# Performance work log

Hardware: AMD Instinct MI355X
Metric: run time of the kernel (lower is better)

The kernel has to match this reference:

```python
import math
import jax, jax.numpy as jnp
import numpy as np

# ---- hyperparams (match init_kwargs) ----
N_LEVELS = 16
F = 2                      # n_features_per_level
LOG2_T = 19                # log2_hashmap_size
BASE_RES = 16
PER_LEVEL_SCALE = 1.5
N_POINTS = 2 ** 21


def _aligned_level_size(res):
    return min(((res * res + 7) // 8) * 8, 1 << LOG2_T)

# static per-level resolution / offset tables (Python ints, mirror torch __init__)
RES, OFFS = [], []
_off = 0
_log2s = math.log2(PER_LEVEL_SCALE)
for _l in range(N_LEVELS):
    _scale = 2.0 ** (_l * _log2s) * BASE_RES - 1.0
    _r = int(math.ceil(_scale) + 1)
    RES.append(_r)
    OFFS.append(_off)
    _off += _aligned_level_size(_r)
TOTAL = _off
SIZES = [(OFFS[l + 1] - OFFS[l]) if l + 1 < N_LEVELS else TOTAL - OFFS[l]
         for l in range(N_LEVELS)]


def setup_inputs() -> dict:
    key = jax.random.key(0)
    k1, k2 = jax.random.split(key)
    # scale to [0, 0.95) so all 4 corner indices stay in-range on dense levels
    xy = jax.random.uniform(k1, (N_POINTS, 2), jnp.float32) * 0.95
    params = jax.random.uniform(k2, (TOTAL * F,), jnp.float32,
                                minval=-1e-4, maxval=1e-4)
    return {"xy": xy, "params": params}


def _grid_index(gx, gy, res, hsize):
    if hsize >= res * res:            # dense level
        return gx + gy * res
    # coherent prime hash in uint32 arithmetic (wraps == & 0xFFFFFFFF)
    h = (gx.astype(jnp.uint32) ^ (gy.astype(jnp.uint32) * jnp.uint32(2654435761)))
    return (h % jnp.uint32(hsize)).astype(jnp.int32)


def reference(xy, params):
    table = params.reshape(TOTAL, F)          # [TOTAL, F]
    outs = []
    for l in range(N_LEVELS):                 # small static loop over levels
        res, off, hsize = RES[l], OFFS[l], SIZES[l]
        pos = xy * (res - 1.0) + 0.5          # [N, 2]
        pg = jnp.floor(pos)
        frac = pos - pg
        pg = pg.astype(jnp.int32)
        gx0, gy0 = pg[:, 0], pg[:, 1]
        gx1, gy1 = gx0 + 1, gy0 + 1
        wx, wy = frac[:, 0:1], frac[:, 1:2]   # [N, 1]
        i00 = off + _grid_index(gx0, gy0, res, hsize)
        i10 = off + _grid_index(gx1, gy0, res, hsize)
        i01 = off + _grid_index(gx0, gy1, res, hsize)
        i11 = off + _grid_index(gx1, gy1, res, hsize)
        f00 = jnp.take(table, i00, axis=0)    # [N, F]
        f10 = jnp.take(table, i10, axis=0)
        f01 = jnp.take(table, i01, axis=0)
        f11 = jnp.take(table, i11, axis=0)
        out_l = (f00 * ((1.0 - wx) * (1.0 - wy))
                 + f10 * (wx * (1.0 - wy))
                 + f01 * ((1.0 - wx) * wy)
                 + f11 * (wx * wy))
        outs.append(out_l)
    return jnp.concatenate(outs, axis=-1)     # [N, N_LEVELS * F]
```

## Files before the change

kernel.cpp:

```cpp
#include <hip/hip_runtime.h>
#include <math.h>

#define N_LEVELS 16
#define NPTS (1 << 21)

typedef float vfloat4 __attribute__((ext_vector_type(4)));
typedef float vfloat2 __attribute__((ext_vector_type(2)));

struct LevelP {
    float scale;
    int   res;
    int   off;
    unsigned int mask;
    int   is_hash;
};
struct LevelTable { LevelP lv[N_LEVELS]; };
struct LevelMap   { int m[8][2]; };

__global__ __launch_bounds__(256) void enc_level_kernel(
        const float2* __restrict__ xy,
        const float*  __restrict__ table,
        float2* __restrict__ ws,
        LevelTable lt, LevelMap lm)
{
    int xcd   = blockIdx.x & 7;
    int slot  = blockIdx.x >> 3;
    int lvl   = lm.m[xcd][slot >> 10];
    int chunk = slot & 1023;

    const LevelP lp = lt.lv[lvl];
    const float2* tb = (const float2*)table + lp.off;
    float2* wsl = ws + (size_t)lvl * NPTS;

    int base = chunk * 2048 + threadIdx.x;

    #pragma unroll
    for (int i = 0; i < 8; ++i) {
        int p = base + i * 256;
        float2 pt = xy[p];

        float px = __fadd_rn(__fmul_rn(pt.x, lp.scale), 0.5f);
        float py = __fadd_rn(__fmul_rn(pt.y, lp.scale), 0.5f);
        float fx = floorf(px), fy = floorf(py);
        float wx = __fsub_rn(px, fx), wy = __fsub_rn(py, fy);
        int gx = (int)fx, gy = (int)fy;

        int i00, i10, i01, i11;
        if (lp.is_hash) {
            const unsigned K1 = 2654435761u;
            unsigned ux = (unsigned)gx, uy = (unsigned)gy;
            unsigned hy0 = uy * K1, hy1 = (uy + 1u) * K1;
            i00 = (int)((ux        ^ hy0) & lp.mask);
            i10 = (int)(((ux + 1u) ^ hy0) & lp.mask);
            i01 = (int)((ux        ^ hy1) & lp.mask);
            i11 = (int)(((ux + 1u) ^ hy1) & lp.mask);
        } else {
            i00 = gx + gy * lp.res;
            i10 = i00 + 1;
            i01 = i00 + lp.res;
            i11 = i01 + 1;
        }

        float2 f00 = tb[i00];
        float2 f10 = tb[i10];
        float2 f01 = tb[i01];
        float2 f11 = tb[i11];

        float owx = 1.0f - wx, owy = 1.0f - wy;
        float w00 = owx * owy, w10 = wx * owy, w01 = owx * wy, w11 = wx * wy;
        vfloat2 o;
        o.x = f00.x * w00 + f10.x * w10 + f01.x * w01 + f11.x * w11;
        o.y = f00.y * w00 + f10.y * w10 + f01.y * w01 + f11.y * w11;

        __builtin_nontemporal_store(o, (vfloat2*)&wsl[p]);
    }
}

__global__ __launch_bounds__(256) void interleave_kernel(
        const float2* __restrict__ ws,
        float4* __restrict__ out)
{
    int tid  = blockIdx.x * 256 + threadIdx.x;
    int pair = tid & 7;
    int p    = tid >> 3;

    const vfloat2* a = (const vfloat2*)(ws + (size_t)(2 * pair)     * NPTS);
    const vfloat2* b = (const vfloat2*)(ws + (size_t)(2 * pair + 1) * NPTS);
    vfloat2 va = __builtin_nontemporal_load(&a[p]);
    vfloat2 vb = __builtin_nontemporal_load(&b[p]);

    vfloat4 o = { va.x, va.y, vb.x, vb.y };
    __builtin_nontemporal_store(o, (vfloat4*)&out[(size_t)p * 8 + pair]);
}

__global__ __launch_bounds__(256) void hashenc_kernel(
        const float2* __restrict__ xy,
        const float*  __restrict__ table,
        float4* __restrict__ out,
        LevelTable lt)
{
    int tid  = blockIdx.x * 256 + threadIdx.x;
    int pair = tid & 7;
    int p    = tid >> 3;

    float2 pt = xy[p];
    float4 o;

    #pragma unroll
    for (int k = 0; k < 2; ++k) {
        const LevelP lp = lt.lv[2 * pair + k];
        float px = __fadd_rn(__fmul_rn(pt.x, lp.scale), 0.5f);
        float py = __fadd_rn(__fmul_rn(pt.y, lp.scale), 0.5f);
        float fx = floorf(px), fy = floorf(py);
        float wx = __fsub_rn(px, fx), wy = __fsub_rn(py, fy);
        int gx = (int)fx, gy = (int)fy;

        int i00, i10, i01, i11;
        if (lp.is_hash) {
            const unsigned K1 = 2654435761u;
            unsigned ux = (unsigned)gx, uy = (unsigned)gy;
            unsigned hy0 = uy * K1, hy1 = (uy + 1u) * K1;
            i00 = (int)((ux        ^ hy0) & lp.mask);
            i10 = (int)(((ux + 1u) ^ hy0) & lp.mask);
            i01 = (int)((ux        ^ hy1) & lp.mask);
            i11 = (int)(((ux + 1u) ^ hy1) & lp.mask);
        } else {
            i00 = gx + gy * lp.res;
            i10 = i00 + 1;
            i01 = i00 + lp.res;
            i11 = i01 + 1;
        }

        const float2* tb = (const float2*)table + lp.off;
        float2 f00 = tb[i00];
        float2 f10 = tb[i10];
        float2 f01 = tb[i01];
        float2 f11 = tb[i11];

        float owx = 1.0f - wx, owy = 1.0f - wy;
        float w00 = owx * owy, w10 = wx * owy, w01 = owx * wy, w11 = wx * wy;
        float ox = f00.x * w00 + f10.x * w10 + f01.x * w01 + f11.x * w11;
        float oy = f00.y * w00 + f10.y * w10 + f01.y * w01 + f11.y * w11;

        if (k == 0) { o.x = ox; o.y = oy; }
        else        { o.z = ox; o.w = oy; }
    }

    vfloat4 ov = { o.x, o.y, o.z, o.w };
    __builtin_nontemporal_store(ov, (vfloat4*)&out[(size_t)p * 8 + pair]);
}

extern "C" void kernel_launch(void* const* d_in, const int* in_sizes, int n_in,
                              void* d_out, int out_size, void* d_ws, size_t ws_size,
                              hipStream_t stream) {
    const float2* xy     = (const float2*)d_in[0];
    const float*  params = (const float*)d_in[1];
    float4*       out    = (float4*)d_out;

    LevelTable lt;
    double log2s = log2(1.5);
    long offs[N_LEVELS];
    int  res_arr[N_LEVELS];
    long off = 0;
    for (int l = 0; l < N_LEVELS; ++l) {
        double scale = pow(2.0, (double)l * log2s) * 16.0 - 1.0;
        int r = (int)ceil(scale) + 1;
        res_arr[l] = r;
        offs[l] = off;
        long sz = ((long)r * r + 7) / 8 * 8;
        if (sz > (1L << 19)) sz = 1L << 19;
        off += sz;
    }
    for (int l = 0; l < N_LEVELS; ++l) {
        long hsize = ((l + 1 < N_LEVELS) ? offs[l + 1] : off) - offs[l];
        long r2 = (long)res_arr[l] * res_arr[l];
        int is_hash = hsize < r2;
        lt.lv[l].scale   = (float)(res_arr[l] - 1);
        lt.lv[l].res     = res_arr[l];
        lt.lv[l].off     = (int)offs[l];
        lt.lv[l].is_hash = is_hash;
        lt.lv[l].mask    = is_hash ? (unsigned)(hsize - 1) : 0u;
    }

    size_t ws_needed = (size_t)N_LEVELS * NPTS * 2 * sizeof(float);
    if (ws_size >= ws_needed) {
        LevelMap lm;
        int map[8][2] = { {10,0},{11,1},{12,2},{13,3},{14,4},{15,5},{6,7},{8,9} };
        for (int x = 0; x < 8; ++x) { lm.m[x][0] = map[x][0]; lm.m[x][1] = map[x][1]; }

        float2* ws = (float2*)d_ws;
        dim3 gridA(16384), block(256);
        hipLaunchKernelGGL(enc_level_kernel, gridA, block, 0, stream,
                           xy, params, ws, lt, lm);
        dim3 gridB((NPTS * 8) / 256);
        hipLaunchKernelGGL(interleave_kernel, gridB, block, 0, stream,
                           (const float2*)ws, out);
    } else {
        long total_threads = (long)NPTS * 8;
        dim3 grid((unsigned)(total_threads / 256)), block(256);
        hipLaunchKernelGGL(hashenc_kernel, grid, block, 0, stream,
                           xy, params, out, lt);
    }
}
```

Measured before the change: 771.7 us.

## Batch gathers in encoder and stage interleave through LDS with coalesced loads

The per-level encoder now computes indices for four points at a time, then issues all sixteen table gathers before interpolating, which raises memory-level parallelism per thread. The interleave kernel now has each block read 256 points for all 16 levels with coalesced loads into padded shared memory, then write the interleaved output contiguously. The old version used strided 8-byte reads per thread. The encoder change costs more registers, which may reduce occupancy, and the interleave change adds an LDS round trip and a barrier.

After: 698.3 us. 1.11x faster.

```diff
diff --git a/kernel.cpp b/kernel.cpp
--- a/kernel.cpp
+++ b/kernel.cpp
@@ -35,10 +35,105 @@
     int base = chunk * 2048 + threadIdx.x;
 
     #pragma unroll
-    for (int i = 0; i < 8; ++i) {
-        int p = base + i * 256;
-        float2 pt = xy[p];
-
+    for (int half = 0; half < 2; ++half) {
+
+        float wxs[4], wys[4];
+        int   idx[4][4];
+        #pragma unroll
+        for (int i = 0; i < 4; ++i) {
+            int p = base + half * 1024 + i * 256;
+            float2 pt = xy[p];
+
+            float px = __fadd_rn(__fmul_rn(pt.x, lp.scale), 0.5f);
+            float py = __fadd_rn(__fmul_rn(pt.y, lp.scale), 0.5f);
+            float fx = floorf(px), fy = floorf(py);
+            wxs[i] = __fsub_rn(px, fx);
+            wys[i] = __fsub_rn(py, fy);
+            int gx = (int)fx, gy = (int)fy;
+
+            if (lp.is_hash) {
+                const unsigned K1 = 2654435761u;
+                unsigned ux = (unsigned)gx, uy = (unsigned)gy;
+                unsigned hy0 = uy * K1, hy1 = (uy + 1u) * K1;
+                idx[i][0] = (int)((ux        ^ hy0) & lp.mask);
+                idx[i][1] = (int)(((ux + 1u) ^ hy0) & lp.mask);
+                idx[i][2] = (int)((ux        ^ hy1) & lp.mask);
+                idx[i][3] = (int)(((ux + 1u) ^ hy1) & lp.mask);
+            } else {
+                int i00 = gx + gy * lp.res;
+                idx[i][0] = i00;
+                idx[i][1] = i00 + 1;
+                idx[i][2] = i00 + lp.res;
+                idx[i][3] = i00 + lp.res + 1;
+            }
+        }
+
+        float2 f[4][4];
+        #pragma unroll
+        for (int i = 0; i < 4; ++i)
+            #pragma unroll
+            for (int c = 0; c < 4; ++c)
+                f[i][c] = tb[idx[i][c]];
+
+        #pragma unroll
+        for (int i = 0; i < 4; ++i) {
+            float wx = wxs[i], wy = wys[i];
+            float owx = 1.0f - wx, owy = 1.0f - wy;
+            float w00 = owx * owy, w10 = wx * owy, w01 = owx * wy, w11 = wx * wy;
+            vfloat2 o;
+            o.x = f[i][0].x * w00 + f[i][1].x * w10 + f[i][2].x * w01 + f[i][3].x * w11;
+            o.y = f[i][0].y * w00 + f[i][1].y * w10 + f[i][2].y * w01 + f[i][3].y * w11;
+            int p = base + half * 1024 + i * 256;
+            __builtin_nontemporal_store(o, (vfloat2*)&wsl[p]);
+        }
+    }
+}
+
+#define ROWP 258
+__global__ __launch_bounds__(256) void interleave_kernel(
+        const float2* __restrict__ ws,
+        float4* __restrict__ out)
+{
+    __shared__ float2 lds[N_LEVELS * ROWP];
+
+    int t = threadIdx.x;
+    int pbase = blockIdx.x * 256;
+
+    #pragma unroll
+    for (int l = 0; l < N_LEVELS; ++l) {
+        vfloat2 v = __builtin_nontemporal_load(
+            (const vfloat2*)&ws[(size_t)l * NPTS + pbase + t]);
+        lds[l * ROWP + t] = float2{ v.x, v.y };
+    }
+    __syncthreads();
+
+    #pragma unroll
+    for (int w = 0; w < 8; ++w) {
+        int s = w * 256 + t;
+        int p = s >> 3, k = s & 7;
+        float2 a = lds[(2 * k)     * ROWP + p];
+        float2 b = lds[(2 * k + 1) * ROWP + p];
+        vfloat4 o = { a.x, a.y, b.x, b.y };
+        __builtin_nontemporal_store(o, (vfloat4*)&out[(size_t)pbase * 8 + s]);
+    }
+}
+
+__global__ __launch_bounds__(256) void hashenc_kernel(
+        const float2* __restrict__ xy,
+        const float*  __restrict__ table,
+        float4* __restrict__ out,
+        LevelTable lt)
+{
+    int tid  = blockIdx.x * 256 + threadIdx.x;
+    int pair = tid & 7;
+    int p    = tid >> 3;
+
+    float2 pt = xy[p];
+    float4 o;
+
+    #pragma unroll
+    for (int k = 0; k < 2; ++k) {
+        const LevelP lp = lt.lv[2 * pair + k];
         float px = __fadd_rn(__fmul_rn(pt.x, lp.scale), 0.5f);
         float py = __fadd_rn(__fmul_rn(pt.y, lp.scale), 0.5f);
         float fx = floorf(px), fy = floorf(py);
@@ -61,76 +156,6 @@
             i11 = i01 + 1;
         }
 
-        float2 f00 = tb[i00];
-        float2 f10 = tb[i10];
-        float2 f01 = tb[i01];
-        float2 f11 = tb[i11];
-
-        float owx = 1.0f - wx, owy = 1.0f - wy;
-        float w00 = owx * owy, w10 = wx * owy, w01 = owx * wy, w11 = wx * wy;
-        vfloat2 o;
-        o.x = f00.x * w00 + f10.x * w10 + f01.x * w01 + f11.x * w11;
-        o.y = f00.y * w00 + f10.y * w10 + f01.y * w01 + f11.y * w11;
-
-        __builtin_nontemporal_store(o, (vfloat2*)&wsl[p]);
-    }
-}
-
-__global__ __launch_bounds__(256) void interleave_kernel(
-        const float2* __restrict__ ws,
-        float4* __restrict__ out)
-{
-    int tid  = blockIdx.x * 256 + threadIdx.x;
-    int pair = tid & 7;
-    int p    = tid >> 3;
-
-    const vfloat2* a = (const vfloat2*)(ws + (size_t)(2 * pair)     * NPTS);
-    const vfloat2* b = (const vfloat2*)(ws + (size_t)(2 * pair + 1) * NPTS);
-    vfloat2 va = __builtin_nontemporal_load(&a[p]);
-    vfloat2 vb = __builtin_nontemporal_load(&b[p]);
-
-    vfloat4 o = { va.x, va.y, vb.x, vb.y };
-    __builtin_nontemporal_store(o, (vfloat4*)&out[(size_t)p * 8 + pair]);
-}
-
-__global__ __launch_bounds__(256) void hashenc_kernel(
-        const float2* __restrict__ xy,
-        const float*  __restrict__ table,
-        float4* __restrict__ out,
-        LevelTable lt)
-{
-    int tid  = blockIdx.x * 256 + threadIdx.x;
-    int pair = tid & 7;
-    int p    = tid >> 3;
-
-    float2 pt = xy[p];
-    float4 o;
-
-    #pragma unroll
-    for (int k = 0; k < 2; ++k) {
-        const LevelP lp = lt.lv[2 * pair + k];
-        float px = __fadd_rn(__fmul_rn(pt.x, lp.scale), 0.5f);
-        float py = __fadd_rn(__fmul_rn(pt.y, lp.scale), 0.5f);
-        float fx = floorf(px), fy = floorf(py);
-        float wx = __fsub_rn(px, fx), wy = __fsub_rn(py, fy);
-        int gx = (int)fx, gy = (int)fy;
-
-        int i00, i10, i01, i11;
-        if (lp.is_hash) {
-            const unsigned K1 = 2654435761u;
-            unsigned ux = (unsigned)gx, uy = (unsigned)gy;
-            unsigned hy0 = uy * K1, hy1 = (uy + 1u) * K1;
-            i00 = (int)((ux        ^ hy0) & lp.mask);
-            i10 = (int)(((ux + 1u) ^ hy0) & lp.mask);
-            i01 = (int)((ux        ^ hy1) & lp.mask);
-            i11 = (int)(((ux + 1u) ^ hy1) & lp.mask);
-        } else {
-            i00 = gx + gy * lp.res;
-            i10 = i00 + 1;
-            i01 = i00 + lp.res;
-            i11 = i01 + 1;
-        }
-
         const float2* tb = (const float2*)table + lp.off;
         float2 f00 = tb[i00];
         float2 f10 = tb[i10];
@@ -192,7 +217,7 @@
         dim3 gridA(16384), block(256);
         hipLaunchKernelGGL(enc_level_kernel, gridA, block, 0, stream,
                            xy, params, ws, lt, lm);
-        dim3 gridB((NPTS * 8) / 256);
+        dim3 gridB(NPTS / 256);
         hipLaunchKernelGGL(interleave_kernel, gridB, block, 0, stream,
                            (const float2*)ws, out);
     } else {
```
